# Kernel tuning notes

Measured on AMD Instinct MI355X. Metric: run time of the kernel, lower is better.

The kernel has to match this reference:

```python
import jax, jax.numpy as jnp
import numpy as np

B, S, HID = 4, 1024, 1024
H = 16
D = HID // H  # 64
SPARSITY = 0.9  # keep prob = 0.1


def setup_inputs() -> dict:
    key = jax.random.key(0)
    ks = jax.random.split(key, 11)
    sc = 1.0 / np.sqrt(HID)
    x = jax.random.normal(ks[0], (B, S, HID), dtype=jnp.float32)
    Wq = jax.random.normal(ks[1], (HID, HID), dtype=jnp.float32) * sc
    bq = jnp.zeros((HID,), dtype=jnp.float32)
    Wk = jax.random.normal(ks[2], (HID, HID), dtype=jnp.float32) * sc
    bk = jnp.zeros((HID,), dtype=jnp.float32)
    Wv = jax.random.normal(ks[3], (HID, HID), dtype=jnp.float32) * sc
    bv = jnp.zeros((HID,), dtype=jnp.float32)
    Wo = jax.random.normal(ks[4], (HID, HID), dtype=jnp.float32) * sc
    bo = jnp.zeros((HID,), dtype=jnp.float32)
    temperature = jnp.ones((H, 1, 1), dtype=jnp.float32)
    # training-mode random sparsity mask: rand > sparsity -> keep (True)
    sparse_mask = jax.random.uniform(ks[5], (B, H, S, S)) > SPARSITY
    return {"x": x, "Wq": Wq, "bq": bq, "Wk": Wk, "bk": bk, "Wv": Wv,
            "bv": bv, "Wo": Wo, "bo": bo, "temperature": temperature,
            "sparse_mask": sparse_mask}


def reference(x, Wq, bq, Wk, bk, Wv, bv, Wo, bo, temperature, sparse_mask):
    b, s, _ = x.shape
    def split_heads(t):
        return t.reshape(b, s, H, D).transpose(0, 2, 1, 3)  # [B,H,S,D]
    q = split_heads(x @ Wq + bq)
    k = split_heads(x @ Wk + bk)
    v = split_heads(x @ Wv + bv)
    scores = jnp.einsum('bhqd,bhkd->bhqk', q, k) / np.sqrt(D)
    scores = scores * temperature  # [H,1,1] broadcasts over [B,H,S,S]
    scores = jnp.where(sparse_mask, scores, -jnp.inf)
    attn = jax.nn.softmax(scores, axis=-1)
    out = jnp.einsum('bhqk,bhkd->bhqd', attn, v)
    out = out.transpose(0, 2, 1, 3).reshape(b, s, HID)
    return out @ Wo + bo
```

## Files before the change

### kernel.cpp

```cpp
#include <hip/hip_runtime.h>

typedef unsigned short u16;
typedef short short8 __attribute__((ext_vector_type(8)));
typedef float f32x4 __attribute__((ext_vector_type(4)));
typedef float float4v __attribute__((ext_vector_type(4)));
typedef u16 u16x4 __attribute__((ext_vector_type(4)));
typedef unsigned uint2v __attribute__((ext_vector_type(2)));
typedef unsigned long long u64;

__device__ __forceinline__ u16 f2bf(float f) {
  union { float f; unsigned u; } v; v.f = f;
  unsigned r = v.u + 0x7FFFu + ((v.u >> 16) & 1u);
  return (u16)(r >> 16);
}

__device__ __forceinline__ unsigned cvtpk(float lo, float hi) {
  unsigned r;
  asm("v_cvt_pk_bf16_f32 %0, %1, %2" : "=v"(r) : "v"(lo), "v"(hi));
  return r;
}

__device__ __forceinline__ void gload16(const u16* g, u16* l) {
  __builtin_amdgcn_global_load_lds(
      (const __attribute__((address_space(1))) void*)g,
      (__attribute__((address_space(3))) void*)l, 16, 0, 0);
}

union PackSS { unsigned u[4]; short8 s; };

__global__ __launch_bounds__(256)
void prep_kernel(const void* __restrict__ mask, u64* __restrict__ bits,
                 const float* __restrict__ x, u16* __restrict__ xb,
                 const float* __restrict__ W0, const float* __restrict__ W1,
                 const float* __restrict__ W2, const float* __restrict__ W3,
                 u16* __restrict__ Wt) {
  __shared__ float t[32][33];
  __shared__ int sf;
  const int bid = blockIdx.x;
  if (bid < 4096) {
    if (threadIdx.x == 0) sf = 0;
    __syncthreads();
    {
      uint4 v = ((const uint4*)mask)[threadIdx.x];
      unsigned xs[4] = {v.x, v.y, v.z, v.w};
      int f = 0;
#pragma unroll
      for (int d = 0; d < 4; ++d) {
        unsigned u = xs[d];
        if (u == 0x3F800000u) f |= 1;
        if (u & 0xFFFFFF00u) f |= 2;
        if ((d & 1) && u) f |= 4;
      }
      if (f) atomicOr(&sf, f);
    }
    __syncthreads();
    const int fl = sf;
    const int fmt = (fl & 1) ? 2 : ((fl & 2) ? 0 : ((fl & 4) ? 1 : 3));

    const int wi = bid * 256 + threadIdx.x;
    u64 b = 0;
    if (fmt == 0) {
      const uint4* mp = (const uint4*)mask + (size_t)wi * 4;
#pragma unroll
      for (int i = 0; i < 4; ++i) {
        uint4 v = mp[i];
        unsigned xw[4] = {v.x, v.y, v.z, v.w};
#pragma unroll
        for (int d = 0; d < 4; ++d)
#pragma unroll
          for (int by = 0; by < 4; ++by)
            if (xw[d] & (0xFFu << (by * 8))) b |= 1ULL << (i * 16 + d * 4 + by);
      }
    } else if (fmt != 3) {
      const uint4* mp = (const uint4*)mask + (size_t)wi * 16;
#pragma unroll
      for (int i = 0; i < 16; ++i) {
        uint4 v = mp[i];
        if (v.x) b |= 1ULL << (i * 4 + 0);
        if (v.y) b |= 1ULL << (i * 4 + 1);
        if (v.z) b |= 1ULL << (i * 4 + 2);
        if (v.w) b |= 1ULL << (i * 4 + 3);
      }
    } else {
      const uint4* mp = (const uint4*)mask + (size_t)wi * 32;
#pragma unroll
      for (int i = 0; i < 32; ++i) {
        uint4 v = mp[i];
        if (v.x | v.y) b |= 1ULL << (i * 2 + 0);
        if (v.z | v.w) b |= 1ULL << (i * 2 + 1);
      }
    }
    int bh = wi >> 14, q = (wi >> 4) & 1023, kt = wi & 15;
    bits[((size_t)bh * 16 + kt) * 1024 + q] = b;
  } else if (bid < 8192) {
    int i = ((bid - 4096) * 256 + threadIdx.x) * 4;
    float4v v = *(const float4v*)(x + i);
    u16x4 o;
    o[0] = f2bf(v[0]); o[1] = f2bf(v[1]); o[2] = f2bf(v[2]); o[3] = f2bf(v[3]);
    *(u16x4*)(xb + i) = o;
  } else {
    int i = bid - 8192;
    int z = i >> 10, rest = i & 1023;
    const float* W = (z == 0) ? W0 : (z == 1) ? W1 : (z == 2) ? W2 : W3;
    u16* out = Wt + (size_t)z * 1024 * 1024;
    int n0 = (rest & 31) * 32, k0 = (rest >> 5) * 32;
    int tx = threadIdx.x & 31, ty = threadIdx.x >> 5;
#pragma unroll
    for (int j = 0; j < 4; ++j)
      t[ty + 8 * j][tx] = W[(size_t)(k0 + ty + 8 * j) * 1024 + n0 + tx];
    __syncthreads();
#pragma unroll
    for (int j = 0; j < 4; ++j)
      out[(size_t)(n0 + ty + 8 * j) * 1024 + k0 + tx] = f2bf(t[tx][ty + 8 * j]);
  }
}

template<int BN>
__global__ __launch_bounds__(256)
void gemm_kernel(const u16* __restrict__ A,
                 const u16* __restrict__ Bt0, const u16* __restrict__ Bt1, const u16* __restrict__ Bt2,
                 const float* __restrict__ b0, const float* __restrict__ b1, const float* __restrict__ b2,
                 const float* __restrict__ temp,
                 u16* __restrict__ qb, u16* __restrict__ kb, u16* __restrict__ vT,
                 float* __restrict__ fo, int phase) {
  constexpr int K = 1024;
  constexpr int WN = BN / 2;
  constexpr int NC = WN / 16;
  __shared__ u16 As[128 * 32];
  __shared__ u16 Bs[BN * 32];
  const int tid = threadIdx.x;
  const int lane = tid & 63, w = tid >> 6;
  const int l15 = lane & 15, l4 = lane >> 4;
  const int m0 = blockIdx.x * 128, n0 = blockIdx.y * BN;
  const int z = blockIdx.z;
  const u16* Bt = (z == 0) ? Bt0 : (z == 1) ? Bt1 : Bt2;
  const float* bias = (z == 0) ? b0 : (z == 1) ? b1 : b2;
  const int wr = w >> 1, wc = w & 1;

  f32x4 acc[4][NC] = {};

  const int c0 = tid, c1 = 256 + tid;
  const u16* ga0 = A + (size_t)(m0 + (c0 >> 2)) * K + (c0 & 3) * 8;
  const u16* ga1 = A + (size_t)(m0 + (c1 >> 2)) * K + (c1 & 3) * 8;
  const u16* gb0 = Bt + (size_t)(n0 + (c0 >> 2)) * K + (c0 & 3) * 8;
  const u16* gb1 = Bt + (size_t)(n0 + (c1 >> 2)) * K + (c1 & 3) * 8;
  u16* la0 = As + c0 * 8;
  u16* la1 = As + c1 * 8;
  u16* lb0 = Bs + c0 * 8;
  u16* lb1 = Bs + c1 * 8;

  for (int kt = 0; kt < K; kt += 32) {
    gload16(ga0 + kt, la0);
    gload16(ga1 + kt, la1);
    gload16(gb0 + kt, lb0);
    if (BN == 128) gload16(gb1 + kt, lb1);
    __syncthreads();
    short8 af[4], bfr[NC];
#pragma unroll
    for (int r = 0; r < 4; ++r)
      af[r] = *(const short8*)(As + (wr * 64 + r * 16 + l15) * 32 + l4 * 8);
#pragma unroll
    for (int c = 0; c < NC; ++c)
      bfr[c] = *(const short8*)(Bs + (wc * WN + c * 16 + l15) * 32 + l4 * 8);
#pragma unroll
    for (int r = 0; r < 4; ++r)
#pragma unroll
      for (int c = 0; c < NC; ++c)
        acc[r][c] = __builtin_amdgcn_mfma_f32_16x16x32_bf16(bfr[c], af[r], acc[r][c], 0, 0, 0);
    __syncthreads();
  }

  float bvj[NC][4];
#pragma unroll
  for (int c = 0; c < NC; ++c)
#pragma unroll
    for (int j = 0; j < 4; ++j)
      bvj[c][j] = bias[n0 + wc * WN + c * 16 + l4 * 4 + j];
  const float fac = (phase == 0 && z == 0)
      ? temp[(n0 + wc * WN) >> 6] * 0.18033688011112042f : 1.0f;

#pragma unroll
  for (int r = 0; r < 4; ++r) {
    const int mm = m0 + wr * 64 + r * 16 + l15;
    const int b = mm >> 10, s = mm & 1023;
#pragma unroll
    for (int c = 0; c < NC; ++c) {
      const int n = n0 + wc * WN + c * 16 + l4 * 4;
      if (phase == 1) {
        float4v o;
#pragma unroll
        for (int j = 0; j < 4; ++j) o[j] = acc[r][c][j] + bvj[c][j];
        *(float4v*)(fo + (size_t)mm * 1024 + n) = o;
      } else if (z == 2) {
#pragma unroll
        for (int j = 0; j < 4; ++j)
          vT[((size_t)b * 1024 + n + j) * 1024 + s] = f2bf(acc[r][c][j] + bvj[c][j]);
      } else {
        unsigned lo = cvtpk((acc[r][c][0] + bvj[c][0]) * fac, (acc[r][c][1] + bvj[c][1]) * fac);
        unsigned hi = cvtpk((acc[r][c][2] + bvj[c][2]) * fac, (acc[r][c][3] + bvj[c][3]) * fac);
        unsigned o2[2] = {lo, hi};
        int hh = n >> 6, d = n & 63;
        u16* dst = (z == 0) ? qb : kb;
        *(unsigned long long*)(dst + ((((size_t)b * 16 + hh) * 1024 + s) * 64 + d)) =
            *(unsigned long long*)o2;
      }
    }
  }
}

__global__ __launch_bounds__(512, 4)
void attn_kernel(const u16* __restrict__ qb, const u16* __restrict__ kb, const u16* __restrict__ vT,
                 const u64* __restrict__ mbits, u16* __restrict__ oh) {
  __shared__ u16 Ks[2][64 * 64];
  __shared__ u16 Vs[2][64 * 64];
  const int tid = threadIdx.x, lane = tid & 63, w = tid >> 6;
  const int l15 = lane & 15, l4 = lane >> 4;
  const int id = blockIdx.x;
  const int xcd = id & 7, sl = id >> 3;
  const int bh = xcd * 8 + (sl >> 3), qx = sl & 7;
  const int b = bh >> 4, h = bh & 15;
  const int q0 = qx * 128 + w * 16;
  const u16* qp = qb + ((size_t)bh * 1024 + q0) * 64;
  const u16* kp = kb + (size_t)bh * 1024 * 64;
  const u16* vp = vT + (size_t)bh * 64 * 1024;

  const int sr = tid >> 3, sc = ((tid & 7) ^ (sr & 7)) * 8;
  const int swz8 = (l15 & 7) << 3;
  const int vswz = l15 & 7;

  short8 qf0 = *(const short8*)(qp + (size_t)l15 * 64 + l4 * 8);
  short8 qf1 = *(const short8*)(qp + (size_t)l15 * 64 + 32 + l4 * 8);

  float m = -1e30f, l = 0.f;
  f32x4 oacc[4] = {};

  const u64* mb = mbits + (size_t)bh * 16 * 1024 + q0 + l15;
  u64 wcur = mb[0];

  gload16(kp + (size_t)sr * 64 + sc, &Ks[0][tid * 8]);
  gload16(vp + (size_t)sr * 1024 + sc, &Vs[0][tid * 8]);

  for (int t = 0; t < 16; ++t) {
    const int buf = t & 1;
    __syncthreads();

    if (t < 15) {
      const int k1 = (t + 1) * 64;
      gload16(kp + (size_t)(k1 + sr) * 64 + sc, &Ks[buf ^ 1][tid * 8]);
      gload16(vp + (size_t)sr * 1024 + k1 + sc, &Vs[buf ^ 1][tid * 8]);
    }
    u64 wnext = (t < 15) ? mb[(t + 1) * 1024] : 0ULL;

    f32x4 s[4] = {};
    __builtin_amdgcn_s_setprio(1);
#pragma unroll
    for (int cb = 0; cb < 4; ++cb) {
      const u16* kr = &Ks[buf][(cb * 16 + l15) * 64];
      short8 kf0 = *(const short8*)(kr + ((l4 * 8) ^ swz8));
      short8 kf1 = *(const short8*)(kr + ((32 + l4 * 8) ^ swz8));
      s[cb] = __builtin_amdgcn_mfma_f32_16x16x32_bf16(kf0, qf0, s[cb], 0, 0, 0);
      s[cb] = __builtin_amdgcn_mfma_f32_16x16x32_bf16(kf1, qf1, s[cb], 0, 0, 0);
    }
    __builtin_amdgcn_s_setprio(0);

    float mt = fmaxf(fmaxf(s[0][0], s[0][1]), fmaxf(s[0][2], s[0][3]));
#pragma unroll
    for (int cb = 1; cb < 4; ++cb)
      mt = fmaxf(mt, fmaxf(fmaxf(s[cb][0], s[cb][1]), fmaxf(s[cb][2], s[cb][3])));
    mt = fmaxf(mt, __shfl_xor(mt, 16));
    mt = fmaxf(mt, __shfl_xor(mt, 32));
    if (!__all(mt <= m + 8.f)) {
      float mnew = fmaxf(m, mt);
      float al = exp2f(m - mnew);
      l *= al;
#pragma unroll
      for (int db = 0; db < 4; ++db) oacc[db] *= al;
      m = mnew;
    }
    unsigned hws[4] = {(unsigned)wcur, (unsigned)(wcur >> 16),
                       (unsigned)(wcur >> 32), (unsigned)(wcur >> 48)};
    float rs = 0.f;
#pragma unroll
    for (int cb = 0; cb < 4; ++cb) {
#pragma unroll
      for (int j = 0; j < 4; ++j) {
        float p = exp2f(s[cb][j] - m);
        p = ((hws[cb] >> (l4 * 4 + j)) & 1) ? p : 0.f;
        rs += p;
        s[cb][j] = p;
      }
    }
    rs += __shfl_xor(rs, 16);
    rs += __shfl_xor(rs, 32);
    l += rs;

    PackSS pb0, pb1;
    pb0.u[0] = cvtpk(s[0][0], s[0][1]); pb0.u[1] = cvtpk(s[0][2], s[0][3]);
    pb0.u[2] = cvtpk(s[1][0], s[1][1]); pb0.u[3] = cvtpk(s[1][2], s[1][3]);
    pb1.u[0] = cvtpk(s[2][0], s[2][1]); pb1.u[1] = cvtpk(s[2][2], s[2][3]);
    pb1.u[2] = cvtpk(s[3][0], s[3][1]); pb1.u[3] = cvtpk(s[3][2], s[3][3]);

    __builtin_amdgcn_s_setprio(1);
#pragma unroll
    for (int kg = 0; kg < 2; ++kg) {
#pragma unroll
      for (int db = 0; db < 4; ++db) {
        const u16* vrow = &Vs[buf][(db * 16 + l15) * 64];
        const int e0 = (((4 * kg + (l4 >> 1)) ^ vswz) << 3) + (l4 & 1) * 4;
        const int e1 = (((4 * kg + 2 + (l4 >> 1)) ^ vswz) << 3) + (l4 & 1) * 4;
        uint2v v0 = *(const uint2v*)(vrow + e0);
        uint2v v1 = *(const uint2v*)(vrow + e1);
        PackSS vf;
        vf.u[0] = v0[0]; vf.u[1] = v0[1]; vf.u[2] = v1[0]; vf.u[3] = v1[1];
        oacc[db] = __builtin_amdgcn_mfma_f32_16x16x32_bf16(
            vf.s, kg ? pb1.s : pb0.s, oacc[db], 0, 0, 0);
      }
    }
    __builtin_amdgcn_s_setprio(0);
    wcur = wnext;
  }

  float rl = 1.f / l;
  u16* orow = oh + ((size_t)b * 1024 + q0 + l15) * 1024 + h * 64;
#pragma unroll
  for (int db = 0; db < 4; ++db) {
    unsigned a0 = cvtpk(oacc[db][0] * rl, oacc[db][1] * rl);
    unsigned a1 = cvtpk(oacc[db][2] * rl, oacc[db][3] * rl);
    unsigned oA[2] = {a0, a1};
    *(unsigned long long*)(orow + db * 16 + l4 * 4) = *(unsigned long long*)oA;
  }
}

extern "C" void kernel_launch(void* const* d_in, const int* in_sizes, int n_in,
                              void* d_out, int out_size, void* d_ws, size_t ws_size,
                              hipStream_t stream) {
  const float* x = (const float*)d_in[0];
  const float* Wq = (const float*)d_in[1];
  const float* bq = (const float*)d_in[2];
  const float* Wk = (const float*)d_in[3];
  const float* bk = (const float*)d_in[4];
  const float* Wv = (const float*)d_in[5];
  const float* bv = (const float*)d_in[6];
  const float* Wo = (const float*)d_in[7];
  const float* bo = (const float*)d_in[8];
  const float* temp = (const float*)d_in[9];
  const void* mask = (const void*)d_in[10];

  char* ws = (char*)d_ws;
  u16* xb = (u16*)(ws + 256);
  u16* Wt = xb + (size_t)4 * 1024 * 1024;
  u16* qbuf = Wt + (size_t)4 * 1024 * 1024;
  u16* kbuf = qbuf + (size_t)4 * 1024 * 1024;
  u16* vTb = kbuf + (size_t)4 * 1024 * 1024;
  u64* mbits = (u64*)(vTb + (size_t)4 * 1024 * 1024);
  u16* oh = xb;

  prep_kernel<<<12288, 256, 0, stream>>>(mask, mbits, x, xb, Wq, Wk, Wv, Wo, Wt);
  gemm_kernel<128><<<dim3(32, 8, 3), 256, 0, stream>>>(
      xb, Wt, Wt + 1024 * 1024, Wt + 2 * 1024 * 1024,
      bq, bk, bv, temp, qbuf, kbuf, vTb, nullptr, 0);
  attn_kernel<<<512, 512, 0, stream>>>(qbuf, kbuf, vTb, mbits, oh);
  gemm_kernel<64><<<dim3(32, 16, 1), 256, 0, stream>>>(
      oh, Wt + 3 * 1024 * 1024, nullptr, nullptr,
      bo, nullptr, nullptr, temp, nullptr, nullptr, nullptr, (float*)d_out, 1);
}
```

Measured before the change: 188.4 us.

## Deepen GEMM K-tiles with swizzled LDS, shrink attention blocks, coalesce mask reads

The QKV and output-projection GEMMs are split into dedicated kernels that use a 64-wide K step with XOR-swizzled shared-memory layout, halving the number of barriers and reducing LDS bank conflicts. The attention kernel drops to 256 threads per block, each covering 64 queries, and doubles the grid to 1024 blocks for better occupancy and load balance, with each thread loading two chunks of K/V. The mask-bit prep kernel is re-indexed so output writes are contiguous while input reads are strided. Larger LDS tiles per GEMM block may lower occupancy.

After: 195.7 us. 3.9% more time.

```diff
diff --git a/kernel.cpp b/kernel.cpp
--- a/kernel.cpp
+++ b/kernel.cpp
@@ -58,9 +58,10 @@
     const int fmt = (fl & 1) ? 2 : ((fl & 2) ? 0 : ((fl & 4) ? 1 : 3));
 
     const int wi = bid * 256 + threadIdx.x;
+    const int bh = wi >> 14, kt = (wi >> 10) & 15, q = wi & 1023;
     u64 b = 0;
     if (fmt == 0) {
-      const uint4* mp = (const uint4*)mask + (size_t)wi * 4;
+      const uint4* mp = (const uint4*)mask + (((size_t)bh << 16) + (q << 6) + (kt << 2));
 #pragma unroll
       for (int i = 0; i < 4; ++i) {
         uint4 v = mp[i];
@@ -72,7 +73,7 @@
             if (xw[d] & (0xFFu << (by * 8))) b |= 1ULL << (i * 16 + d * 4 + by);
       }
     } else if (fmt != 3) {
-      const uint4* mp = (const uint4*)mask + (size_t)wi * 16;
+      const uint4* mp = (const uint4*)mask + (((size_t)bh << 18) + (q << 8) + (kt << 4));
 #pragma unroll
       for (int i = 0; i < 16; ++i) {
         uint4 v = mp[i];
@@ -82,7 +83,7 @@
         if (v.w) b |= 1ULL << (i * 4 + 3);
       }
     } else {
-      const uint4* mp = (const uint4*)mask + (size_t)wi * 32;
+      const uint4* mp = (const uint4*)mask + (((size_t)bh << 19) + (q << 9) + (kt << 5));
 #pragma unroll
       for (int i = 0; i < 32; ++i) {
         uint4 v = mp[i];
@@ -90,8 +91,7 @@
         if (v.z | v.w) b |= 1ULL << (i * 2 + 1);
       }
     }
-    int bh = wi >> 14, q = (wi >> 4) & 1023, kt = wi & 15;
-    bits[((size_t)bh * 16 + kt) * 1024 + q] = b;
+    bits[wi] = b;
   } else if (bid < 8192) {
     int i = ((bid - 4096) * 256 + threadIdx.x) * 4;
     float4v v = *(const float4v*)(x + i);
@@ -102,7 +102,7 @@
     int i = bid - 8192;
     int z = i >> 10, rest = i & 1023;
     const float* W = (z == 0) ? W0 : (z == 1) ? W1 : (z == 2) ? W2 : W3;
-    u16* out = Wt + (size_t)z * 1024 * 1024;
+    u16* outw = Wt + (size_t)z * 1048576;
     int n0 = (rest & 31) * 32, k0 = (rest >> 5) * 32;
     int tx = threadIdx.x & 31, ty = threadIdx.x >> 5;
 #pragma unroll
@@ -111,87 +111,79 @@
     __syncthreads();
 #pragma unroll
     for (int j = 0; j < 4; ++j)
-      out[(size_t)(n0 + ty + 8 * j) * 1024 + k0 + tx] = f2bf(t[tx][ty + 8 * j]);
-  }
-}
-
-template<int BN>
+      outw[(size_t)(n0 + ty + 8 * j) * 1024 + k0 + tx] = f2bf(t[tx][ty + 8 * j]);
+  }
+}
+
 __global__ __launch_bounds__(256)
-void gemm_kernel(const u16* __restrict__ A,
-                 const u16* __restrict__ Bt0, const u16* __restrict__ Bt1, const u16* __restrict__ Bt2,
-                 const float* __restrict__ b0, const float* __restrict__ b1, const float* __restrict__ b2,
-                 const float* __restrict__ temp,
-                 u16* __restrict__ qb, u16* __restrict__ kb, u16* __restrict__ vT,
-                 float* __restrict__ fo, int phase) {
-  constexpr int K = 1024;
-  constexpr int WN = BN / 2;
-  constexpr int NC = WN / 16;
-  __shared__ u16 As[128 * 32];
-  __shared__ u16 Bs[BN * 32];
-  const int tid = threadIdx.x;
-  const int lane = tid & 63, w = tid >> 6;
+void qkv_kernel(const u16* __restrict__ A, const u16* __restrict__ Wt,
+                const float* __restrict__ b0, const float* __restrict__ b1,
+                const float* __restrict__ b2, const float* __restrict__ temp,
+                u16* __restrict__ qb, u16* __restrict__ kb, u16* __restrict__ vT) {
+  __shared__ u16 As[128 * 64];
+  __shared__ u16 Bs[128 * 64];
+  const int tid = threadIdx.x, lane = tid & 63, w = tid >> 6;
   const int l15 = lane & 15, l4 = lane >> 4;
-  const int m0 = blockIdx.x * 128, n0 = blockIdx.y * BN;
+  const int m0 = blockIdx.x * 128, n0 = blockIdx.y * 128;
   const int z = blockIdx.z;
-  const u16* Bt = (z == 0) ? Bt0 : (z == 1) ? Bt1 : Bt2;
+  const u16* Bt = Wt + (size_t)z * 1048576;
   const float* bias = (z == 0) ? b0 : (z == 1) ? b1 : b2;
   const int wr = w >> 1, wc = w & 1;
 
-  f32x4 acc[4][NC] = {};
-
-  const int c0 = tid, c1 = 256 + tid;
-  const u16* ga0 = A + (size_t)(m0 + (c0 >> 2)) * K + (c0 & 3) * 8;
-  const u16* ga1 = A + (size_t)(m0 + (c1 >> 2)) * K + (c1 & 3) * 8;
-  const u16* gb0 = Bt + (size_t)(n0 + (c0 >> 2)) * K + (c0 & 3) * 8;
-  const u16* gb1 = Bt + (size_t)(n0 + (c1 >> 2)) * K + (c1 & 3) * 8;
-  u16* la0 = As + c0 * 8;
-  u16* la1 = As + c1 * 8;
-  u16* lb0 = Bs + c0 * 8;
-  u16* lb1 = Bs + c1 * 8;
-
-  for (int kt = 0; kt < K; kt += 32) {
-    gload16(ga0 + kt, la0);
-    gload16(ga1 + kt, la1);
-    gload16(gb0 + kt, lb0);
-    if (BN == 128) gload16(gb1 + kt, lb1);
-    __syncthreads();
-    short8 af[4], bfr[NC];
-#pragma unroll
-    for (int r = 0; r < 4; ++r)
-      af[r] = *(const short8*)(As + (wr * 64 + r * 16 + l15) * 32 + l4 * 8);
-#pragma unroll
-    for (int c = 0; c < NC; ++c)
-      bfr[c] = *(const short8*)(Bs + (wc * WN + c * 16 + l15) * 32 + l4 * 8);
-#pragma unroll
-    for (int r = 0; r < 4; ++r)
-#pragma unroll
-      for (int c = 0; c < NC; ++c)
-        acc[r][c] = __builtin_amdgcn_mfma_f32_16x16x32_bf16(bfr[c], af[r], acc[r][c], 0, 0, 0);
-    __syncthreads();
-  }
-
-  float bvj[NC][4];
-#pragma unroll
-  for (int c = 0; c < NC; ++c)
+  f32x4 acc[4][4] = {};
+
+  int arow[4], acg[4];
+#pragma unroll
+  for (int i = 0; i < 4; ++i) {
+    int c = tid + 256 * i;
+    arow[i] = c >> 3; acg[i] = ((c & 7) ^ (arow[i] & 7)) * 8;
+  }
+
+  for (int kt = 0; kt < 1024; kt += 64) {
+#pragma unroll
+    for (int i = 0; i < 4; ++i) {
+      gload16(A + (size_t)(m0 + arow[i]) * 1024 + kt + acg[i], As + (tid + 256 * i) * 8);
+      gload16(Bt + (size_t)(n0 + arow[i]) * 1024 + kt + acg[i], Bs + (tid + 256 * i) * 8);
+    }
+    __syncthreads();
+#pragma unroll
+    for (int kk = 0; kk < 2; ++kk) {
+      short8 af[4], bf[4];
+#pragma unroll
+      for (int r = 0; r < 4; ++r) {
+        int row = wr * 64 + r * 16 + l15;
+        af[r] = *(const short8*)(As + row * 64 + (((kk * 4 + l4) ^ (row & 7)) * 8));
+      }
+#pragma unroll
+      for (int c = 0; c < 4; ++c) {
+        int row = wc * 64 + c * 16 + l15;
+        bf[c] = *(const short8*)(Bs + row * 64 + (((kk * 4 + l4) ^ (row & 7)) * 8));
+      }
+#pragma unroll
+      for (int r = 0; r < 4; ++r)
+#pragma unroll
+        for (int c = 0; c < 4; ++c)
+          acc[r][c] = __builtin_amdgcn_mfma_f32_16x16x32_bf16(bf[c], af[r], acc[r][c], 0, 0, 0);
+    }
+    __syncthreads();
+  }
+
+  float bvj[4][4];
+#pragma unroll
+  for (int c = 0; c < 4; ++c)
 #pragma unroll
     for (int j = 0; j < 4; ++j)
-      bvj[c][j] = bias[n0 + wc * WN + c * 16 + l4 * 4 + j];
-  const float fac = (phase == 0 && z == 0)
-      ? temp[(n0 + wc * WN) >> 6] * 0.18033688011112042f : 1.0f;
+      bvj[c][j] = bias[n0 + wc * 64 + c * 16 + l4 * 4 + j];
+  const float fac = (z == 0) ? temp[(n0 + wc * 64) >> 6] * 0.18033688011112042f : 1.0f;
 
 #pragma unroll
   for (int r = 0; r < 4; ++r) {
     const int mm = m0 + wr * 64 + r * 16 + l15;
     const int b = mm >> 10, s = mm & 1023;
 #pragma unroll
-    for (int c = 0; c < NC; ++c) {
-      const int n = n0 + wc * WN + c * 16 + l4 * 4;
-      if (phase == 1) {
-        float4v o;
-#pragma unroll
-        for (int j = 0; j < 4; ++j) o[j] = acc[r][c][j] + bvj[c][j];
-        *(float4v*)(fo + (size_t)mm * 1024 + n) = o;
-      } else if (z == 2) {
+    for (int c = 0; c < 4; ++c) {
+      const int n = n0 + wc * 64 + c * 16 + l4 * 4;
+      if (z == 2) {
 #pragma unroll
         for (int j = 0; j < 4; ++j)
           vT[((size_t)b * 1024 + n + j) * 1024 + s] = f2bf(acc[r][c][j] + bvj[c][j]);
@@ -208,23 +200,26 @@
   }
 }
 
-__global__ __launch_bounds__(512, 4)
-void attn_kernel(const u16* __restrict__ qb, const u16* __restrict__ kb, const u16* __restrict__ vT,
-                 const u64* __restrict__ mbits, u16* __restrict__ oh) {
+__global__ __launch_bounds__(256, 4)
+void attn_kernel(const u16* __restrict__ qb, const u16* __restrict__ kb,
+                 const u16* __restrict__ vT, const u64* __restrict__ mbits,
+                 u16* __restrict__ oh) {
   __shared__ u16 Ks[2][64 * 64];
   __shared__ u16 Vs[2][64 * 64];
   const int tid = threadIdx.x, lane = tid & 63, w = tid >> 6;
   const int l15 = lane & 15, l4 = lane >> 4;
   const int id = blockIdx.x;
-  const int xcd = id & 7, sl = id >> 3;
-  const int bh = xcd * 8 + (sl >> 3), qx = sl & 7;
+  const int xcd = id & 7, rest = id >> 3;
+  const int bh = xcd * 8 + (rest & 7), qx = rest >> 3;
   const int b = bh >> 4, h = bh & 15;
-  const int q0 = qx * 128 + w * 16;
+  const int q0 = qx * 64 + w * 16;
   const u16* qp = qb + ((size_t)bh * 1024 + q0) * 64;
   const u16* kp = kb + (size_t)bh * 1024 * 64;
   const u16* vp = vT + (size_t)bh * 64 * 1024;
 
-  const int sr = tid >> 3, sc = ((tid & 7) ^ (sr & 7)) * 8;
+  const int L0 = tid, L1 = tid + 256;
+  const int r0 = L0 >> 3, c0 = ((L0 & 7) ^ (r0 & 7)) * 8;
+  const int r1 = L1 >> 3, c1 = ((L1 & 7) ^ (r1 & 7)) * 8;
   const int swz8 = (l15 & 7) << 3;
   const int vswz = l15 & 7;
 
@@ -237,8 +232,10 @@
   const u64* mb = mbits + (size_t)bh * 16 * 1024 + q0 + l15;
   u64 wcur = mb[0];
 
-  gload16(kp + (size_t)sr * 64 + sc, &Ks[0][tid * 8]);
-  gload16(vp + (size_t)sr * 1024 + sc, &Vs[0][tid * 8]);
+  gload16(kp + (size_t)r0 * 64 + c0, &Ks[0][L0 * 8]);
+  gload16(kp + (size_t)r1 * 64 + c1, &Ks[0][L1 * 8]);
+  gload16(vp + (size_t)r0 * 1024 + c0, &Vs[0][L0 * 8]);
+  gload16(vp + (size_t)r1 * 1024 + c1, &Vs[0][L1 * 8]);
 
   for (int t = 0; t < 16; ++t) {
     const int buf = t & 1;
@@ -246,8 +243,10 @@
 
     if (t < 15) {
       const int k1 = (t + 1) * 64;
-      gload16(kp + (size_t)(k1 + sr) * 64 + sc, &Ks[buf ^ 1][tid * 8]);
-      gload16(vp + (size_t)sr * 1024 + k1 + sc, &Vs[buf ^ 1][tid * 8]);
+      gload16(kp + (size_t)(k1 + r0) * 64 + c0, &Ks[buf ^ 1][L0 * 8]);
+      gload16(kp + (size_t)(k1 + r1) * 64 + c1, &Ks[buf ^ 1][L1 * 8]);
+      gload16(vp + (size_t)r0 * 1024 + k1 + c0, &Vs[buf ^ 1][L0 * 8]);
+      gload16(vp + (size_t)r1 * 1024 + k1 + c1, &Vs[buf ^ 1][L1 * 8]);
     }
     u64 wnext = (t < 15) ? mb[(t + 1) * 1024] : 0ULL;
 
@@ -328,6 +327,76 @@
     unsigned a1 = cvtpk(oacc[db][2] * rl, oacc[db][3] * rl);
     unsigned oA[2] = {a0, a1};
     *(unsigned long long*)(orow + db * 16 + l4 * 4) = *(unsigned long long*)oA;
+  }
+}
+
+__global__ __launch_bounds__(256)
+void oproj_kernel(const u16* __restrict__ A, const u16* __restrict__ Bt,
+                  const float* __restrict__ bias, float* __restrict__ fo) {
+  __shared__ u16 As[128 * 64];
+  __shared__ u16 Bs[64 * 64];
+  const int tid = threadIdx.x, lane = tid & 63, w = tid >> 6;
+  const int l15 = lane & 15, l4 = lane >> 4;
+  const int m0 = blockIdx.x * 128, n0 = blockIdx.y * 64;
+  const int wr = w >> 1, wc = w & 1;
+
+  f32x4 acc[4][2] = {};
+
+  int arow[4], acg[4];
+#pragma unroll
+  for (int i = 0; i < 4; ++i) {
+    int c = tid + 256 * i;
+    arow[i] = c >> 3; acg[i] = ((c & 7) ^ (arow[i] & 7)) * 8;
+  }
+
+  for (int kt = 0; kt < 1024; kt += 64) {
+#pragma unroll
+    for (int i = 0; i < 4; ++i)
+      gload16(A + (size_t)(m0 + arow[i]) * 1024 + kt + acg[i], As + (tid + 256 * i) * 8);
+#pragma unroll
+    for (int i = 0; i < 2; ++i)
+      gload16(Bt + (size_t)(n0 + arow[i]) * 1024 + kt + acg[i], Bs + (tid + 256 * i) * 8);
+    __syncthreads();
+#pragma unroll
+    for (int kk = 0; kk < 2; ++kk) {
+      short8 af[4], bf[2];
+#pragma unroll
+      for (int r = 0; r < 4; ++r) {
+        int row = wr * 64 + r * 16 + l15;
+        af[r] = *(const short8*)(As + row * 64 + (((kk * 4 + l4) ^ (row & 7)) * 8));
+      }
+#pragma unroll
+      for (int c = 0; c < 2; ++c) {
+        int row = wc * 32 + c * 16 + l15;
+        bf[c] = *(const short8*)(Bs + row * 64 + (((kk * 4 + l4) ^ (row & 7)) * 8));
+      }
+#pragma unroll
+      for (int r = 0; r < 4; ++r)
+#pragma unroll
+        for (int c = 0; c < 2; ++c)
+          acc[r][c] = __builtin_amdgcn_mfma_f32_16x16x32_bf16(bf[c], af[r], acc[r][c], 0, 0, 0);
+    }
+    __syncthreads();
+  }
+
+  float bvj[2][4];
+#pragma unroll
+  for (int c = 0; c < 2; ++c)
+#pragma unroll
+    for (int j = 0; j < 4; ++j)
+      bvj[c][j] = bias[n0 + wc * 32 + c * 16 + l4 * 4 + j];
+
+#pragma unroll
+  for (int r = 0; r < 4; ++r) {
+    const int mm = m0 + wr * 64 + r * 16 + l15;
+#pragma unroll
+    for (int c = 0; c < 2; ++c) {
+      const int n = n0 + wc * 32 + c * 16 + l4 * 4;
+      float4v o;
+#pragma unroll
+      for (int j = 0; j < 4; ++j) o[j] = acc[r][c][j] + bvj[c][j];
+      *(float4v*)(fo + (size_t)mm * 1024 + n) = o;
+    }
   }
 }
 
@@ -356,11 +425,9 @@
   u16* oh = xb;
 
   prep_kernel<<<12288, 256, 0, stream>>>(mask, mbits, x, xb, Wq, Wk, Wv, Wo, Wt);
-  gemm_kernel<128><<<dim3(32, 8, 3), 256, 0, stream>>>(
-      xb, Wt, Wt + 1024 * 1024, Wt + 2 * 1024 * 1024,
-      bq, bk, bv, temp, qbuf, kbuf, vTb, nullptr, 0);
-  attn_kernel<<<512, 512, 0, stream>>>(qbuf, kbuf, vTb, mbits, oh);
-  gemm_kernel<64><<<dim3(32, 16, 1), 256, 0, stream>>>(
-      oh, Wt + 3 * 1024 * 1024, nullptr, nullptr,
-      bo, nullptr, nullptr, temp, nullptr, nullptr, nullptr, (float*)d_out, 1);
-}
+  qkv_kernel<<<dim3(32, 8, 3), 256, 0, stream>>>(
+      xb, Wt, bq, bk, bv, temp, qbuf, kbuf, vTb);
+  attn_kernel<<<1024, 256, 0, stream>>>(qbuf, kbuf, vTb, mbits, oh);
+  oproj_kernel<<<dim3(32, 16), 256, 0, stream>>>(
+      oh, Wt + (size_t)3 * 1048576, bo, (float*)d_out);
+}
```
